# Performance work log

Hardware: AMD Instinct MI355X
Metric: run time of the kernel (lower is better)

The kernel has to match this reference:

```python
import jax, jax.numpy as jnp
import numpy as np

B, S, D = 8, 1024, 1024
H = 16
HD = D // H  # 64
FF = 4 * D   # 4096
EPS = 1e-5


def layer_norm(x, g, b):
    mu = jnp.mean(x, axis=-1, keepdims=True)
    var = jnp.mean(jnp.square(x - mu), axis=-1, keepdims=True)
    return (x - mu) * jax.lax.rsqrt(var + EPS) * g + b


def setup_inputs() -> dict:
    key = jax.random.key(0)
    ks = jax.random.split(key, 16)
    s_in = 1.0 / np.sqrt(D)
    s_ff = 1.0 / np.sqrt(FF)
    return {
        "x": jax.random.normal(ks[0], (B, S, D), jnp.float32),
        "ln1_g": jnp.ones((D,), jnp.float32),
        "ln1_b": jnp.zeros((D,), jnp.float32),
        "ln2_g": jnp.ones((D,), jnp.float32),
        "ln2_b": jnp.zeros((D,), jnp.float32),
        # per-head projections stacked on a leading head axis: [H, D, HD]
        "Wq": jax.random.uniform(ks[1], (H, D, HD), jnp.float32, -s_in, s_in),
        "bq": jax.random.uniform(ks[2], (H, HD), jnp.float32, -s_in, s_in),
        "Wk": jax.random.uniform(ks[3], (H, D, HD), jnp.float32, -s_in, s_in),
        "bk": jax.random.uniform(ks[4], (H, HD), jnp.float32, -s_in, s_in),
        "Wv": jax.random.uniform(ks[5], (H, D, HD), jnp.float32, -s_in, s_in),
        "bv": jax.random.uniform(ks[6], (H, HD), jnp.float32, -s_in, s_in),
        "Wo": jax.random.uniform(ks[7], (D, D), jnp.float32, -s_in, s_in),
        "bo": jax.random.uniform(ks[8], (D,), jnp.float32, -s_in, s_in),
        "W1": jax.random.uniform(ks[9], (D, FF), jnp.float32, -s_in, s_in),
        "b1": jax.random.uniform(ks[10], (FF,), jnp.float32, -s_in, s_in),
        "W2": jax.random.uniform(ks[11], (FF, D), jnp.float32, -s_ff, s_ff),
        "b2": jax.random.uniform(ks[12], (D,), jnp.float32, -s_ff, s_ff),
    }


def attention(h, Wq, bq, Wk, bk, Wv, bv, Wo, bo):
    # h: [B,S,D] -> q/k/v: [B,H,S,HD]
    q = jnp.einsum("bsd,hdk->bhsk", h, Wq) + bq[None, :, None, :]
    k = jnp.einsum("bsd,hdk->bhsk", h, Wk) + bk[None, :, None, :]
    v = jnp.einsum("bsd,hdk->bhsk", h, Wv) + bv[None, :, None, :]
    scores = jnp.einsum("bhsk,bhtk->bhst", q, k) / jnp.sqrt(jnp.float32(HD))
    w = jax.nn.softmax(scores, axis=-1)  # [B,H,S,S]
    o = jnp.einsum("bhst,bhtk->bhsk", w, v)
    # concat heads (head order matches torch.cat over per-head outputs)
    o = o.transpose(0, 2, 1, 3).reshape(h.shape[0], h.shape[1], D)
    return o @ Wo + bo


def reference(x, ln1_g, ln1_b, ln2_g, ln2_b, Wq, bq, Wk, bk, Wv, bv, Wo, bo, W1, b1, W2, b2):
    h = layer_norm(x, ln1_g, ln1_b)
    x = x + attention(h, Wq, bq, Wk, bk, Wv, bv, Wo, bo)
    h2 = layer_norm(x, ln2_g, ln2_b)
    ff = jax.nn.gelu(h2 @ W1 + b1, approximate=False) @ W2 + b2  # dropout in eval = identity
    return x + ff
```

## Files before the change

### kernel.cpp

```cpp
#include <hip/hip_runtime.h>
#include <hip/hip_bf16.h>
#include <math.h>

#define DMODEL 1024
#define NH     16
#define HD     64
#define FFDIM  4096
#define SEQ    1024
#define BATCH  8
#define ROWS   (BATCH * SEQ)

typedef __bf16 bf16x8 __attribute__((ext_vector_type(8)));
typedef __bf16 bf16x4 __attribute__((ext_vector_type(4)));
typedef float  f32x4  __attribute__((ext_vector_type(4)));

__device__ __forceinline__ unsigned short f2bf(float f) {
  unsigned int u = __builtin_bit_cast(unsigned int, f);
  u += 0x7fff + ((u >> 16) & 1);
  return (unsigned short)(u >> 16);
}

__device__ __forceinline__ void gload_lds16(const void* g, void* l) {
  __builtin_amdgcn_global_load_lds(
      (const __attribute__((address_space(1))) unsigned int*)g,
      (__attribute__((address_space(3))) unsigned int*)l, 16, 0, 0);
}

__device__ __forceinline__ bf16x8 tr_read8(const unsigned short* p) {
  bf16x4 lo, hi;
  const __attribute__((address_space(3))) unsigned short* p3 =
      (const __attribute__((address_space(3))) unsigned short*)p;
  asm volatile("ds_read_b64_tr_b16 %0, %2\n\t"
               "ds_read_b64_tr_b16 %1, %2 offset:128"
               : "=v"(lo), "=v"(hi)
               : "v"(p3));
  return __builtin_shufflevector(lo, hi, 0, 1, 2, 3, 4, 5, 6, 7);
}

template <int N>
__device__ __forceinline__ void wait_vm() {
  if constexpr (N == 0)
    asm volatile("s_waitcnt vmcnt(0)" ::: "memory");
  else if constexpr (N == 3)
    asm volatile("s_waitcnt vmcnt(3)" ::: "memory");
  else
    asm volatile("s_waitcnt vmcnt(4)" ::: "memory");
  __builtin_amdgcn_sched_barrier(0);
}

__global__ __launch_bounds__(256) void ln_bf16_kernel(
    const float* __restrict__ x, const float* __restrict__ g,
    const float* __restrict__ bta, unsigned short* __restrict__ out) {
  int row = blockIdx.x;
  int tid = threadIdx.x;
  int wid = tid >> 6, lane = tid & 63;
  const float4 v = ((const float4*)(x + (size_t)row * DMODEL))[tid];
  float s = v.x + v.y + v.z + v.w;
#pragma unroll
  for (int off = 32; off >= 1; off >>= 1) s += __shfl_xor(s, off, 64);
  __shared__ float red[8];
  if (lane == 0) red[wid] = s;
  __syncthreads();
  float mu = (red[0] + red[1] + red[2] + red[3]) * (1.0f / DMODEL);
  float4 d;
  d.x = v.x - mu; d.y = v.y - mu; d.z = v.z - mu; d.w = v.w - mu;
  float sq = d.x * d.x + d.y * d.y + d.z * d.z + d.w * d.w;
#pragma unroll
  for (int off = 32; off >= 1; off >>= 1) sq += __shfl_xor(sq, off, 64);
  if (lane == 0) red[4 + wid] = sq;
  __syncthreads();
  float var = (red[4] + red[5] + red[6] + red[7]) * (1.0f / DMODEL);
  float rs = rsqrtf(var + 1e-5f);
  const float4 gg = ((const float4*)g)[tid];
  const float4 bb = ((const float4*)bta)[tid];
  ushort4 o;
  o.x = f2bf(d.x * rs * gg.x + bb.x);
  o.y = f2bf(d.y * rs * gg.y + bb.y);
  o.z = f2bf(d.z * rs * gg.z + bb.z);
  o.w = f2bf(d.w * rs * gg.w + bb.w);
  ((ushort4*)(out + (size_t)row * DMODEL))[tid] = o;
}

__global__ __launch_bounds__(256) void transpose_f2b_kernel(
    const float* __restrict__ in, unsigned short* __restrict__ out,
    int R, int C, long long ibs, long long obs) {
  __shared__ float tile[64][65];
  int b = blockIdx.z;
  int r0 = blockIdx.y * 64, c0 = blockIdx.x * 64;
  const float* ip = in + (size_t)b * ibs;
  unsigned short* op = out + (size_t)b * obs;
  int tid = threadIdx.x;
  int rl = tid >> 4, cl = (tid & 15) * 4;
#pragma unroll
  for (int it = 0; it < 4; ++it) {
    int r = it * 16 + rl;
    float4 v = *(const float4*)(ip + (size_t)(r0 + r) * C + c0 + cl);
    tile[r][cl] = v.x; tile[r][cl + 1] = v.y;
    tile[r][cl + 2] = v.z; tile[r][cl + 3] = v.w;
  }
  __syncthreads();
#pragma unroll
  for (int it = 0; it < 4; ++it) {
    int c = it * 16 + rl;
    ushort4 o;
    o.x = f2bf(tile[cl + 0][c]); o.y = f2bf(tile[cl + 1][c]);
    o.z = f2bf(tile[cl + 2][c]); o.w = f2bf(tile[cl + 3][c]);
    *(ushort4*)(op + (size_t)(c0 + c) * R + r0 + cl) = o;
  }
}

__global__ __launch_bounds__(256) void transpose_v_kernel(
    const unsigned short* __restrict__ V, unsigned short* __restrict__ Vt) {
  __shared__ unsigned short tile[64][68];
  int bh = blockIdx.y;
  int b = bh >> 4, h = bh & 15;
  int t0 = blockIdx.x * 64;
  int tid = threadIdx.x;
  int rl = tid >> 4, cl = (tid & 15) * 4;
  const unsigned short* ip = V + ((size_t)(b * SEQ + t0)) * DMODEL + h * HD;
#pragma unroll
  for (int it = 0; it < 4; ++it) {
    int t = it * 16 + rl;
    ushort4 v = *(const ushort4*)(ip + (size_t)t * DMODEL + cl);
    tile[t][cl] = v.x; tile[t][cl + 1] = v.y;
    tile[t][cl + 2] = v.z; tile[t][cl + 3] = v.w;
  }
  __syncthreads();
  unsigned short* op = Vt + ((size_t)bh * HD) * SEQ + t0;
#pragma unroll
  for (int it = 0; it < 4; ++it) {
    int d = it * 16 + rl;
    ushort4 o;
    o.x = tile[cl + 0][d]; o.y = tile[cl + 1][d];
    o.z = tile[cl + 2][d]; o.w = tile[cl + 3][d];
    *(ushort4*)(op + (size_t)d * SEQ + cl) = o;
  }
}

#define QSCALE 0.18033688f

template <int BN, int EPI>
__global__ __launch_bounds__(256, (BN == 64) ? 4 : 3) void gemmr3_kernel(
    const unsigned short* __restrict__ A, const unsigned short* __restrict__ Bt,
    const float* __restrict__ bias, const float* __restrict__ bias2,
    const float* __restrict__ bias3, const float* __restrict__ resid,
    unsigned short* __restrict__ outb, unsigned short* __restrict__ outb2,
    unsigned short* __restrict__ outb3, float* __restrict__ outf,
    int M, int N, int K, int NXS) {
  constexpr int NFRAG = BN / 32;
  constexpr int WN = BN / 2;
  constexpr int LPT = (BN == 128) ? 4 : 3;
  constexpr int BSLOT = BN * 64;
  __shared__ __align__(16) unsigned short As[3 * 128 * 32];
  __shared__ __align__(16) unsigned short Bs[3 * BN * 32];

  const int tid = threadIdx.x;
  const int wid = tid >> 6, lane = tid & 63;
  const int l15 = lane & 15, l4 = lane >> 4;
  const int wm = wid >> 1, wn = wid & 1;

  const int id = (int)blockIdx.x;
  const int xcd = id & 7, j = id >> 3;
  const int w = j >> 6, l = j & 63;
  const int spx = (int)gridDim.x >> 9;
  const int g = xcd * spx + w;
  const int by = (g / NXS) * 8 + (l >> 3);
  const int bx = (g % NXS) * 8 + (l & 7);

  const size_t KBY = (size_t)K * 2;

  const int rS = tid >> 2;
  const int cS = ((tid & 3) ^ (rS & 3)) << 4;
  const char* gA = (const char*)A + (size_t)(by * 128 + rS) * KBY + cS;
  const char* gB = (const char*)Bt + (size_t)(bx * BN + rS) * KBY + cS;
  char* sA = (char*)As + tid * 16;
  char* sB = (char*)Bs + tid * 16;

  const int fsw = (l4 ^ (l15 & 3)) << 4;
  const char* aRd = (const char*)As + (wm * 64 + l15) * 64 + fsw;
  const char* bRd = (const char*)Bs + (wn * WN + l15) * 64 + fsw;

  f32x4 acc[4][NFRAG];
  const f32x4 fz = {0.f, 0.f, 0.f, 0.f};
#pragma unroll
  for (int i = 0; i < 4; ++i)
#pragma unroll
    for (int n = 0; n < NFRAG; ++n) acc[i][n] = fz;

  const int nt = K >> 5;

#define STAGE(SLOT, T)                                                       \
  do {                                                                       \
    const size_t ko_ = (size_t)(T) * 64;                                     \
    gload_lds16(gA + ko_, sA + (SLOT) * 8192);                               \
    gload_lds16(gA + 64 * KBY + ko_, sA + (SLOT) * 8192 + 4096);             \
    gload_lds16(gB + ko_, sB + (SLOT) * BSLOT);                              \
    if constexpr (BN == 128)                                                 \
      gload_lds16(gB + 64 * KBY + ko_, sB + (SLOT) * BSLOT + 4096);          \
  } while (0)

  STAGE(0, 0);
  STAGE(1, 1);

  int s = 0;
#pragma unroll 1
  for (int t = 0; t < nt; ++t) {
    if (t + 1 < nt) wait_vm<LPT>(); else wait_vm<0>();
    __builtin_amdgcn_s_barrier();
    __builtin_amdgcn_sched_barrier(0);
    const int s2 = (s == 0) ? 2 : s - 1;
    if (t + 2 < nt) STAGE(s2, t + 2);
    {
      const char* aB = aRd + s * 8192;
      const char* bB = bRd + s * BSLOT;
      bf16x8 av[4], bv[NFRAG];
#pragma unroll
      for (int ni = 0; ni < NFRAG; ++ni) bv[ni] = *(const bf16x8*)(bB + ni * 1024);
#pragma unroll
      for (int mi = 0; mi < 4; ++mi) av[mi] = *(const bf16x8*)(aB + mi * 1024);
      __builtin_amdgcn_s_setprio(1);
#pragma unroll
      for (int mi = 0; mi < 4; ++mi)
#pragma unroll
        for (int ni = 0; ni < NFRAG; ++ni)
          acc[mi][ni] = __builtin_amdgcn_mfma_f32_16x16x32_bf16(
              av[mi], bv[ni], acc[mi][ni], 0, 0, 0);
      __builtin_amdgcn_s_setprio(0);
    }
    s = (s == 2) ? 0 : s + 1;
  }

  if (EPI == 5) {
    const int range = bx >> 3;
    const float* bp = (range == 0) ? bias : (range == 1) ? bias2 : bias3;
    unsigned short* op = (range == 0) ? outb : (range == 1) ? outb2 : outb3;
    const float scale = (range == 0) ? QSCALE : 1.0f;
#pragma unroll
    for (int mi = 0; mi < 4; ++mi) {
#pragma unroll
      for (int ni = 0; ni < NFRAG; ++ni) {
        int colL = (bx & 7) * 128 + wn * WN + ni * 16 + l15;
        float bn = bp[colL];
#pragma unroll
        for (int jj = 0; jj < 4; ++jj) {
          int row = by * 128 + wm * 64 + mi * 16 + l4 * 4 + jj;
          op[(size_t)row * 1024 + colL] = f2bf((acc[mi][ni][jj] + bn) * scale);
        }
      }
    }
  } else {
#pragma unroll
    for (int mi = 0; mi < 4; ++mi) {
#pragma unroll
      for (int ni = 0; ni < NFRAG; ++ni) {
        int col = bx * BN + wn * WN + ni * 16 + l15;
        float bn = bias[col];
#pragma unroll
        for (int jj = 0; jj < 4; ++jj) {
          int row = by * 128 + wm * 64 + mi * 16 + l4 * 4 + jj;
          float v = acc[mi][ni][jj] + bn;
          if (EPI == 1) {
            outf[(size_t)row * N + col] = v + resid[(size_t)row * N + col];
          } else if (EPI == 2) {
            float gel = 0.5f * v * (1.0f + erff(v * 0.70710678118f));
            outb[(size_t)row * N + col] = f2bf(gel);
          } else {
            outb[(size_t)row * N + col] = f2bf(v);
          }
        }
      }
    }
  }
#undef STAGE
}

__global__ __launch_bounds__(256, 3) void attn_kernel(
    const unsigned short* __restrict__ Q, const unsigned short* __restrict__ K,
    const unsigned short* __restrict__ Vt, unsigned short* __restrict__ O) {
  __shared__ __align__(16) unsigned short Ks[128 * 64];
  __shared__ __align__(16) unsigned short Vs[64 * 128];
  __shared__ __align__(16) unsigned short Ps[4][128 * 16];
  int tid = threadIdx.x, wid = tid >> 6, lane = tid & 63;
  int l15 = lane & 15, l4 = lane >> 4;
  int sid = blockIdx.x;
  int aid = (sid & 7) * 256 + (sid >> 3);
  int bh = aid >> 4, qb = aid & 15;
  int b = bh >> 4, h = bh & 15;
  int q0 = qb * 64 + wid * 16;
  const f32x4 fz = {0.f, 0.f, 0.f, 0.f};

  const unsigned short* Qbase = Q + ((size_t)(b * SEQ + q0)) * DMODEL + h * HD;
  bf16x8 qf[2];
#pragma unroll
  for (int kh = 0; kh < 2; ++kh)
    qf[kh] = *(const bf16x8*)(Qbase + (size_t)l15 * DMODEL + kh * 32 + l4 * 8);

  f32x4 o[4];
#pragma unroll
  for (int i = 0; i < 4; ++i) o[i] = fz;
  float mrun[4], lrun[4];
#pragma unroll
  for (int j = 0; j < 4; ++j) { mrun[j] = -1e30f; lrun[j] = 0.0f; }

  const unsigned short* Kb = K + (size_t)b * SEQ * DMODEL + h * HD;
  const unsigned short* Vb = Vt + (size_t)bh * HD * SEQ;
  unsigned short* pbase = &Ps[wid][0];
  int krow = tid >> 3, kchunk = tid & 7;
  int vrow = tid >> 4, vchunk = tid & 15;

  for (int t0 = 0; t0 < SEQ; t0 += 128) {
    __syncthreads();
#pragma unroll
    for (int p = 0; p < 4; ++p) {
      int kr = p * 32 + krow;
      int kg = kchunk ^ (kr & 7);
      gload_lds16(Kb + (size_t)(t0 + kr) * DMODEL + kg * 8,
                  (char*)Ks + p * 4096 + tid * 16);
      int vr = p * 16 + vrow;
      int vg = vchunk ^ (vr & 7);
      gload_lds16(Vb + (size_t)vr * SEQ + t0 + vg * 8,
                  (char*)Vs + p * 4096 + tid * 16);
    }
    __syncthreads();
    f32x4 s[8];
#pragma unroll
    for (int ts = 0; ts < 8; ++ts) {
      int row = ts * 16 + l15;
      bf16x8 k0f = *(const bf16x8*)((const char*)Ks + row * 128 + ((l4) ^ (row & 7)) * 16);
      bf16x8 k1f = *(const bf16x8*)((const char*)Ks + row * 128 + ((4 + l4) ^ (row & 7)) * 16);
      s[ts] = __builtin_amdgcn_mfma_f32_16x16x32_bf16(qf[0], k0f, fz, 0, 0, 0);
      s[ts] = __builtin_amdgcn_mfma_f32_16x16x32_bf16(qf[1], k1f, s[ts], 0, 0, 0);
    }
#pragma unroll
    for (int j = 0; j < 4; ++j) {
      float tm = fmaxf(fmaxf(fmaxf(s[0][j], s[1][j]), fmaxf(s[2][j], s[3][j])),
                       fmaxf(fmaxf(s[4][j], s[5][j]), fmaxf(s[6][j], s[7][j])));
#pragma unroll
      for (int off = 8; off >= 1; off >>= 1) tm = fmaxf(tm, __shfl_xor(tm, off, 16));
      float mnew = fmaxf(mrun[j], tm);
      float alpha = __builtin_amdgcn_exp2f(mrun[j] - mnew);
      float ps = 0.0f;
#pragma unroll
      for (int ts = 0; ts < 8; ++ts) {
        float p = __builtin_amdgcn_exp2f(s[ts][j] - mnew);
        s[ts][j] = p;
        ps += p;
      }
#pragma unroll
      for (int off = 8; off >= 1; off >>= 1) ps += __shfl_xor(ps, off, 16);
      lrun[j] = lrun[j] * alpha + ps;
      mrun[j] = mnew;
#pragma unroll
      for (int d = 0; d < 4; ++d) o[d][j] *= alpha;
    }
#pragma unroll
    for (int ts = 0; ts < 8; ++ts) {
      ushort4 pk;
      pk.x = f2bf(s[ts][0]); pk.y = f2bf(s[ts][1]);
      pk.z = f2bf(s[ts][2]); pk.w = f2bf(s[ts][3]);
      *(ushort4*)((char*)pbase + (ts * 16 + l15) * 32 + l4 * 8) = pk;
    }
    asm volatile("s_waitcnt lgkmcnt(0)" ::: "memory");
    __builtin_amdgcn_sched_barrier(0);
#pragma unroll
    for (int kp = 0; kp < 4; ++kp) {
      bf16x8 pf = tr_read8(pbase + (kp * 32 + l4 * 8) * 16 + l15);
      asm volatile("s_waitcnt lgkmcnt(0)" ::: "memory");
      __builtin_amdgcn_sched_barrier(0);
#pragma unroll
      for (int d = 0; d < 4; ++d) {
        int vr = d * 16 + l15;
        int vphys = (kp * 4 + l4) ^ (vr & 7);
        bf16x8 vf = *(const bf16x8*)((const char*)Vs + vr * 256 + vphys * 16);
        o[d] = __builtin_amdgcn_mfma_f32_16x16x32_bf16(pf, vf, o[d], 0, 0, 0);
      }
    }
  }
  unsigned short* Ob = O + ((size_t)(b * SEQ + q0)) * DMODEL + h * HD;
#pragma unroll
  for (int j = 0; j < 4; ++j) {
    float inv = 1.0f / lrun[j];
#pragma unroll
    for (int d = 0; d < 4; ++d) {
      int row = l4 * 4 + j;
      Ob[(size_t)row * DMODEL + d * 16 + l15] = f2bf(o[d][j] * inv);
    }
  }
}

extern "C" void kernel_launch(void* const* d_in, const int* in_sizes, int n_in,
                              void* d_out, int out_size, void* d_ws, size_t ws_size,
                              hipStream_t stream) {
  (void)in_sizes; (void)n_in; (void)out_size; (void)ws_size;
  const float* x    = (const float*)d_in[0];
  const float* ln1g = (const float*)d_in[1];
  const float* ln1b = (const float*)d_in[2];
  const float* ln2g = (const float*)d_in[3];
  const float* ln2b = (const float*)d_in[4];
  const float* Wq   = (const float*)d_in[5];
  const float* bq   = (const float*)d_in[6];
  const float* Wk   = (const float*)d_in[7];
  const float* bk   = (const float*)d_in[8];
  const float* Wv   = (const float*)d_in[9];
  const float* bv   = (const float*)d_in[10];
  const float* Wo   = (const float*)d_in[11];
  const float* bo   = (const float*)d_in[12];
  const float* W1   = (const float*)d_in[13];
  const float* b1   = (const float*)d_in[14];
  const float* W2   = (const float*)d_in[15];
  const float* b2   = (const float*)d_in[16];
  float* out = (float*)d_out;

  char* ws = (char*)d_ws;
  const size_t MB = 1u << 20;
  unsigned short* wqT = (unsigned short*)(ws + 0 * MB);
  unsigned short* wkT = (unsigned short*)(ws + 2 * MB);
  unsigned short* wvT = (unsigned short*)(ws + 4 * MB);
  unsigned short* woT = (unsigned short*)(ws + 6 * MB);
  unsigned short* w1T = (unsigned short*)(ws + 8 * MB);
  unsigned short* w2T = (unsigned short*)(ws + 16 * MB);
  unsigned short* hb  = (unsigned short*)(ws + 24 * MB);
  unsigned short* Qb  = (unsigned short*)(ws + 40 * MB);
  unsigned short* Kb  = (unsigned short*)(ws + 56 * MB);
  unsigned short* Vb  = (unsigned short*)(ws + 72 * MB);
  unsigned short* Vt  = (unsigned short*)(ws + 88 * MB);
  unsigned short* Ob  = Vb;
  unsigned short* ff1 = (unsigned short*)(ws + 40 * MB);

  transpose_f2b_kernel<<<dim3(1, 16, 16), 256, 0, stream>>>(Wq, wqT, 1024, 64,
                                                            65536LL, 65536LL);
  transpose_f2b_kernel<<<dim3(1, 16, 16), 256, 0, stream>>>(Wk, wkT, 1024, 64,
                                                            65536LL, 65536LL);
  transpose_f2b_kernel<<<dim3(1, 16, 16), 256, 0, stream>>>(Wv, wvT, 1024, 64,
                                                            65536LL, 65536LL);
  transpose_f2b_kernel<<<dim3(16, 16, 1), 256, 0, stream>>>(Wo, woT, 1024, 1024, 0, 0);
  transpose_f2b_kernel<<<dim3(64, 16, 1), 256, 0, stream>>>(W1, w1T, 1024, 4096, 0, 0);
  transpose_f2b_kernel<<<dim3(16, 64, 1), 256, 0, stream>>>(W2, w2T, 4096, 1024, 0, 0);

  ln_bf16_kernel<<<dim3(ROWS), 256, 0, stream>>>(x, ln1g, ln1b, hb);

  gemmr3_kernel<128, 5><<<dim3(1536), 256, 0, stream>>>(
      hb, wqT, bq, bk, bv, nullptr, Qb, Kb, Vb, nullptr, ROWS, 1024, DMODEL, 3);

  transpose_v_kernel<<<dim3(16, 128), 256, 0, stream>>>(Vb, Vt);

  attn_kernel<<<dim3(2048), 256, 0, stream>>>(Qb, Kb, Vt, Ob);

  gemmr3_kernel<64, 1><<<dim3(1024), 256, 0, stream>>>(
      Ob, woT, bo, nullptr, nullptr, x, nullptr, nullptr, nullptr, out,
      ROWS, DMODEL, DMODEL, 2);

  ln_bf16_kernel<<<dim3(ROWS), 256, 0, stream>>>(out, ln2g, ln2b, hb);

  gemmr3_kernel<128, 2><<<dim3(2048), 256, 0, stream>>>(
      hb, w1T, b1, nullptr, nullptr, nullptr, ff1, nullptr, nullptr, nullptr,
      ROWS, FFDIM, DMODEL, 4);

  gemmr3_kernel<64, 1><<<dim3(1024), 256, 0, stream>>>(
      ff1, w2T, b2, nullptr, nullptr, out, nullptr, nullptr, nullptr, out,
      ROWS, DMODEL, FFDIM, 2);
}
```

Baseline: 446.1 us.

## Enlarge GEMM tiles to 256x128 with 8x4 MFMA fragments per wave

Replaces the 128xBN GEMM template with a single 256x128 block tile, giving each wave 128x64 outputs, and adjusts the LDS swizzle, the wait counts and the block-to-tile swizzle mapping. The larger tiles raise arithmetic intensity per LDS and global load and cut the grid size. In exchange register pressure goes up (occupancy bound of 2) and the Wo/W2 GEMMs launch only 256 blocks, which may underfill the GPU's CUs and leave them poorly load-balanced.

```diff
diff --git a/kernel.cpp b/kernel.cpp
--- a/kernel.cpp
+++ b/kernel.cpp
@@ -41,10 +41,8 @@
 __device__ __forceinline__ void wait_vm() {
   if constexpr (N == 0)
     asm volatile("s_waitcnt vmcnt(0)" ::: "memory");
-  else if constexpr (N == 3)
-    asm volatile("s_waitcnt vmcnt(3)" ::: "memory");
   else
-    asm volatile("s_waitcnt vmcnt(4)" ::: "memory");
+    asm volatile("s_waitcnt vmcnt(6)" ::: "memory");
   __builtin_amdgcn_sched_barrier(0);
 }
 
@@ -139,20 +137,16 @@
 
 #define QSCALE 0.18033688f
 
-template <int BN, int EPI>
-__global__ __launch_bounds__(256, (BN == 64) ? 4 : 3) void gemmr3_kernel(
+template <int EPI>
+__global__ __launch_bounds__(256, 2) void gemmw_kernel(
     const unsigned short* __restrict__ A, const unsigned short* __restrict__ Bt,
     const float* __restrict__ bias, const float* __restrict__ bias2,
     const float* __restrict__ bias3, const float* __restrict__ resid,
     unsigned short* __restrict__ outb, unsigned short* __restrict__ outb2,
     unsigned short* __restrict__ outb3, float* __restrict__ outf,
-    int M, int N, int K, int NXS) {
-  constexpr int NFRAG = BN / 32;
-  constexpr int WN = BN / 2;
-  constexpr int LPT = (BN == 128) ? 4 : 3;
-  constexpr int BSLOT = BN * 64;
-  __shared__ __align__(16) unsigned short As[3 * 128 * 32];
-  __shared__ __align__(16) unsigned short Bs[3 * BN * 32];
+    int M, int N, int K, int sc) {
+  __shared__ __align__(16) unsigned short As[3 * 256 * 32];
+  __shared__ __align__(16) unsigned short Bs[3 * 128 * 32];
 
   const int tid = threadIdx.x;
   const int wid = tid >> 6, lane = tid & 63;
@@ -161,42 +155,43 @@
 
   const int id = (int)blockIdx.x;
   const int xcd = id & 7, j = id >> 3;
-  const int w = j >> 6, l = j & 63;
-  const int spx = (int)gridDim.x >> 9;
+  const int w = j >> 3, l = j & 7;
+  const int spx = (int)gridDim.x >> 6;
   const int g = xcd * spx + w;
-  const int by = (g / NXS) * 8 + (l >> 3);
-  const int bx = (g % NXS) * 8 + (l & 7);
+  const int by = g / sc;
+  const int bx = (g % sc) * 8 + l;
 
   const size_t KBY = (size_t)K * 2;
 
   const int rS = tid >> 2;
-  const int cS = ((tid & 3) ^ (rS & 3)) << 4;
-  const char* gA = (const char*)A + (size_t)(by * 128 + rS) * KBY + cS;
-  const char* gB = (const char*)Bt + (size_t)(bx * BN + rS) * KBY + cS;
+  const int cS = ((tid & 3) ^ ((rS >> 1) & 3)) << 4;
+  const char* gA = (const char*)A + (size_t)(by * 256 + rS) * KBY + cS;
+  const char* gB = (const char*)Bt + (size_t)(bx * 128 + rS) * KBY + cS;
   char* sA = (char*)As + tid * 16;
   char* sB = (char*)Bs + tid * 16;
 
-  const int fsw = (l4 ^ (l15 & 3)) << 4;
-  const char* aRd = (const char*)As + (wm * 64 + l15) * 64 + fsw;
-  const char* bRd = (const char*)Bs + (wn * WN + l15) * 64 + fsw;
-
-  f32x4 acc[4][NFRAG];
+  const int fsw = (l4 ^ ((l15 >> 1) & 3)) << 4;
+  const char* aRd = (const char*)As + (wm * 128 + l15) * 64 + fsw;
+  const char* bRd = (const char*)Bs + (wn * 64 + l15) * 64 + fsw;
+
+  f32x4 acc[8][4];
   const f32x4 fz = {0.f, 0.f, 0.f, 0.f};
 #pragma unroll
-  for (int i = 0; i < 4; ++i)
-#pragma unroll
-    for (int n = 0; n < NFRAG; ++n) acc[i][n] = fz;
+  for (int i = 0; i < 8; ++i)
+#pragma unroll
+    for (int n = 0; n < 4; ++n) acc[i][n] = fz;
 
   const int nt = K >> 5;
 
 #define STAGE(SLOT, T)                                                       \
   do {                                                                       \
     const size_t ko_ = (size_t)(T) * 64;                                     \
-    gload_lds16(gA + ko_, sA + (SLOT) * 8192);                               \
-    gload_lds16(gA + 64 * KBY + ko_, sA + (SLOT) * 8192 + 4096);             \
-    gload_lds16(gB + ko_, sB + (SLOT) * BSLOT);                              \
-    if constexpr (BN == 128)                                                 \
-      gload_lds16(gB + 64 * KBY + ko_, sB + (SLOT) * BSLOT + 4096);          \
+    gload_lds16(gA + ko_, sA + (SLOT) * 16384);                              \
+    gload_lds16(gA + 64 * KBY + ko_, sA + (SLOT) * 16384 + 4096);            \
+    gload_lds16(gA + 128 * KBY + ko_, sA + (SLOT) * 16384 + 8192);           \
+    gload_lds16(gA + 192 * KBY + ko_, sA + (SLOT) * 16384 + 12288);          \
+    gload_lds16(gB + ko_, sB + (SLOT) * 8192);                               \
+    gload_lds16(gB + 64 * KBY + ko_, sB + (SLOT) * 8192 + 4096);             \
   } while (0)
 
   STAGE(0, 0);
@@ -205,24 +200,24 @@
   int s = 0;
 #pragma unroll 1
   for (int t = 0; t < nt; ++t) {
-    if (t + 1 < nt) wait_vm<LPT>(); else wait_vm<0>();
+    if (t + 1 < nt) wait_vm<6>(); else wait_vm<0>();
     __builtin_amdgcn_s_barrier();
     __builtin_amdgcn_sched_barrier(0);
     const int s2 = (s == 0) ? 2 : s - 1;
     if (t + 2 < nt) STAGE(s2, t + 2);
     {
-      const char* aB = aRd + s * 8192;
-      const char* bB = bRd + s * BSLOT;
-      bf16x8 av[4], bv[NFRAG];
-#pragma unroll
-      for (int ni = 0; ni < NFRAG; ++ni) bv[ni] = *(const bf16x8*)(bB + ni * 1024);
-#pragma unroll
-      for (int mi = 0; mi < 4; ++mi) av[mi] = *(const bf16x8*)(aB + mi * 1024);
+      const char* aB = aRd + s * 16384;
+      const char* bB = bRd + s * 8192;
+      bf16x8 av[8], bv[4];
+#pragma unroll
+      for (int ni = 0; ni < 4; ++ni) bv[ni] = *(const bf16x8*)(bB + ni * 1024);
+#pragma unroll
+      for (int mi = 0; mi < 8; ++mi) av[mi] = *(const bf16x8*)(aB + mi * 1024);
       __builtin_amdgcn_s_setprio(1);
 #pragma unroll
-      for (int mi = 0; mi < 4; ++mi)
-#pragma unroll
-        for (int ni = 0; ni < NFRAG; ++ni)
+      for (int mi = 0; mi < 8; ++mi)
+#pragma unroll
+        for (int ni = 0; ni < 4; ++ni)
           acc[mi][ni] = __builtin_amdgcn_mfma_f32_16x16x32_bf16(
               av[mi], bv[ni], acc[mi][ni], 0, 0, 0);
       __builtin_amdgcn_s_setprio(0);
@@ -236,28 +231,28 @@
     unsigned short* op = (range == 0) ? outb : (range == 1) ? outb2 : outb3;
     const float scale = (range == 0) ? QSCALE : 1.0f;
 #pragma unroll
-    for (int mi = 0; mi < 4; ++mi) {
-#pragma unroll
-      for (int ni = 0; ni < NFRAG; ++ni) {
-        int colL = (bx & 7) * 128 + wn * WN + ni * 16 + l15;
+    for (int mi = 0; mi < 8; ++mi) {
+#pragma unroll
+      for (int ni = 0; ni < 4; ++ni) {
+        int colL = (bx & 7) * 128 + wn * 64 + ni * 16 + l15;
         float bn = bp[colL];
 #pragma unroll
         for (int jj = 0; jj < 4; ++jj) {
-          int row = by * 128 + wm * 64 + mi * 16 + l4 * 4 + jj;
+          int row = by * 256 + wm * 128 + mi * 16 + l4 * 4 + jj;
           op[(size_t)row * 1024 + colL] = f2bf((acc[mi][ni][jj] + bn) * scale);
         }
       }
     }
   } else {
 #pragma unroll
-    for (int mi = 0; mi < 4; ++mi) {
-#pragma unroll
-      for (int ni = 0; ni < NFRAG; ++ni) {
-        int col = bx * BN + wn * WN + ni * 16 + l15;
+    for (int mi = 0; mi < 8; ++mi) {
+#pragma unroll
+      for (int ni = 0; ni < 4; ++ni) {
+        int col = bx * 128 + wn * 64 + ni * 16 + l15;
         float bn = bias[col];
 #pragma unroll
         for (int jj = 0; jj < 4; ++jj) {
-          int row = by * 128 + wm * 64 + mi * 16 + l4 * 4 + jj;
+          int row = by * 256 + wm * 128 + mi * 16 + l4 * 4 + jj;
           float v = acc[mi][ni][jj] + bn;
           if (EPI == 1) {
             outf[(size_t)row * N + col] = v + resid[(size_t)row * N + col];
@@ -439,24 +434,24 @@
 
   ln_bf16_kernel<<<dim3(ROWS), 256, 0, stream>>>(x, ln1g, ln1b, hb);
 
-  gemmr3_kernel<128, 5><<<dim3(1536), 256, 0, stream>>>(
+  gemmw_kernel<5><<<dim3(768), 256, 0, stream>>>(
       hb, wqT, bq, bk, bv, nullptr, Qb, Kb, Vb, nullptr, ROWS, 1024, DMODEL, 3);
 
   transpose_v_kernel<<<dim3(16, 128), 256, 0, stream>>>(Vb, Vt);
 
   attn_kernel<<<dim3(2048), 256, 0, stream>>>(Qb, Kb, Vt, Ob);
 
-  gemmr3_kernel<64, 1><<<dim3(1024), 256, 0, stream>>>(
+  gemmw_kernel<1><<<dim3(256), 256, 0, stream>>>(
       Ob, woT, bo, nullptr, nullptr, x, nullptr, nullptr, nullptr, out,
-      ROWS, DMODEL, DMODEL, 2);
+      ROWS, DMODEL, DMODEL, 1);
 
   ln_bf16_kernel<<<dim3(ROWS), 256, 0, stream>>>(out, ln2g, ln2b, hb);
 
-  gemmr3_kernel<128, 2><<<dim3(2048), 256, 0, stream>>>(
+  gemmw_kernel<2><<<dim3(1024), 256, 0, stream>>>(
       hb, w1T, b1, nullptr, nullptr, nullptr, ff1, nullptr, nullptr, nullptr,
       ROWS, FFDIM, DMODEL, 4);
 
-  gemmr3_kernel<64, 1><<<dim3(1024), 256, 0, stream>>>(
+  gemmw_kernel<1><<<dim3(256), 256, 0, stream>>>(
       ff1, w2T, b2, nullptr, nullptr, out, nullptr, nullptr, nullptr, out,
-      ROWS, DMODEL, FFDIM, 2);
-}
+      ROWS, DMODEL, FFDIM, 1);
+}
```

After: 487.6 us. 9.3% more time.
